# Optimization experiments

Hardware: AMD Instinct MI355X
Metric: run time of the kernel (lower is better)

The kernel has to match this reference:

```python
import jax, jax.numpy as jnp
import numpy as np


def gat(feat_src, feat_dst, src, dst, W, al, ar, b):
    # DGL GATConv in eval mode: shared fc for src/dst, additive attention,
    # leaky_relu(0.2), edge-softmax per destination node, elu activation, bias.
    H, D = al.shape
    nd = feat_dst.shape[0]
    hs = (feat_src @ W).reshape(-1, H, D)  # [Ns,H,D]
    hd = (feat_dst @ W).reshape(-1, H, D)  # [Nd,H,D]
    el = (hs * al).sum(-1)  # [Ns,H]
    er = (hd * ar).sum(-1)  # [Nd,H]
    e = jax.nn.leaky_relu(el[src] + er[dst], 0.2)  # [E,H]
    m = jax.lax.stop_gradient(jax.ops.segment_max(e, dst, num_segments=nd))
    a = jnp.exp(e - m[dst])
    s = jax.ops.segment_sum(a, dst, num_segments=nd)
    den = s[dst]
    alpha = a / jnp.where(den == 0, 1.0, den)  # allow_zero_in_degree
    rst = jax.ops.segment_sum(alpha[:, :, None] * hs[src], dst, num_segments=nd)
    return jax.nn.elu(rst + b.reshape(H, D))  # [Nd,H,D]


def setup_inputs():
    key = jax.random.key(0)
    ks = jax.random.split(key, 40)
    NP, NQ, NK, NA = 50000, 20000, 30000, 5000
    EM, EQ, EK, EA = 1600000, 200000, 200000, 100000
    IN, ATT, HID, H, OUT = 128, 64, 32, 4, 1000
    w = lambda k, sh: jax.random.normal(k, sh, jnp.float32) * 0.05
    ri = lambda k, e, n: jax.random.randint(k, (e,), 0, n, dtype=jnp.int32)
    d = dict(
        hp=jax.random.normal(ks[0], (NP, IN), jnp.float32),
        hq=jax.random.normal(ks[1], (NQ, ATT), jnp.float32),
        hk=jax.random.normal(ks[2], (NK, ATT), jnp.float32),
        ha=jax.random.normal(ks[3], (NA, ATT), jnp.float32),
        meta_src=ri(ks[4], EM, NP), meta_dst=ri(ks[5], EM, NP),
        q_src=ri(ks[6], EQ, NQ), q_dst=ri(ks[7], EQ, NP),
        k_src=ri(ks[8], EK, NK), k_dst=ri(ks[9], EK, NP),
        a_src=ri(ks[10], EA, NA), a_dst=ri(ks[11], EA, NP),
        W0=w(ks[12], (IN, H * HID)), al0=w(ks[13], (H, HID)), ar0=w(ks[14], (H, HID)), b0=jnp.zeros((H * HID,), jnp.float32),
        W1=w(ks[15], (H * HID, H * HID)), al1=w(ks[16], (H, HID)), ar1=w(ks[17], (H, HID)), b1=jnp.zeros((H * HID,), jnp.float32),
        Wq=w(ks[18], (64, H * 128)), alq=w(ks[19], (H, 128)), arq=w(ks[20], (H, 128)), bq=jnp.zeros((H * 128,), jnp.float32),
        Wkw=w(ks[21], (64, H * 128)), alkw=w(ks[22], (H, 128)), arkw=w(ks[23], (H, 128)), bkw=jnp.zeros((H * 128,), jnp.float32),
        Watt=w(ks[24], (64, H * 128)), alatt=w(ks[25], (H, 128)), aratt=w(ks[26], (H, 128)), batt=jnp.zeros((H * 128,), jnp.float32),
        Wpnn_a=w(ks[27], (IN, 64)), Wpn_a=w(ks[28], (ATT, 64)),
        Wpnn=w(ks[29], (H * HID, 64)), Wpn=w(ks[30], (H * 128, 64)),
        Wpred=w(ks[31], (256, OUT)), bpred=jnp.zeros((OUT,), jnp.float32),
    )
    return d


def reference(hp, hq, hk, ha, meta_src, meta_dst, q_src, q_dst, k_src, k_dst, a_src, a_dst, W0, al0, ar0, b0, W1, al1, ar1, b1, Wq, alq, arq, bq, Wkw, alkw, arkw, bkw, Watt, alatt, aratt, batt, Wpnn_a, Wpn_a, Wpnn, Wpn, Wpred, bpred):
    NP = hp.shape[0]
    # two pnn_layers over the single used metapath graph (index 1 is skipped in the original)
    h = gat(hp, hp, meta_src, meta_dst, W0, al0, ar0, b0).reshape(NP, -1)  # [NP,128]
    h = gat(h, h, meta_src, meta_dst, W1, al1, ar1, b1).reshape(NP, -1)    # [NP,128]
    hpd = hp @ Wpnn_a  # proj_pnn_a(hp_cache) -> dst features for bipartite GATs
    oq = gat(hq @ Wpn_a, hpd, q_src, q_dst, Wq, alq, arq, bq).reshape(NP, -1)      # [NP,512]
    ok = gat(hk @ Wpn_a, hpd, k_src, k_dst, Wkw, alkw, arkw, bkw).reshape(NP, -1)  # [NP,512]
    oa = gat(ha @ Wpn_a, hpd, a_src, a_dst, Watt, alatt, aratt, batt).reshape(NP, -1)  # [NP,512]
    hcat = jnp.concatenate([h @ Wpnn, oq @ Wpn, ok @ Wpn, oa @ Wpn], axis=1)  # [NP,256]
    return hcat @ Wpred + bpred
```

## Files before the change

kernel.cpp:

```cpp
#include <hip/hip_runtime.h>
#include <hip/hip_bf16.h>
#include <math.h>
#include <stdint.h>

typedef __attribute__((ext_vector_type(8))) short bh8;
typedef __attribute__((ext_vector_type(4))) float f32x4;

#define AS1(p) ((const __attribute__((address_space(1))) void*)(p))
#define AS3(p) ((__attribute__((address_space(3))) void*)(p))

__device__ inline ushort f2b(float f){
  uint u = __builtin_bit_cast(uint, f);
  u += 0x7fff + ((u >> 16) & 1);
  return (ushort)(u >> 16);
}
__device__ inline float b2f(ushort b){ return __builtin_bit_cast(float, (uint)b << 16); }

__global__ void fill_zero_i32(int* __restrict__ p, int n){
  int i = blockIdx.x*blockDim.x + threadIdx.x;
  if(i < n) p[i] = 0;
}

struct P4 { const int* src; const int* dst; uint* ebuf; int* cnt; int E; int cap; int bbeg; int bend; };

__global__ __launch_bounds__(256) void partition_all_k(P4 g0, P4 g1, P4 g2, P4 g3,
    int* __restrict__ bcur, int range){
  P4 G; int gi;
  int b = blockIdx.x;
  if(b < g0.bend){ G = g0; gi = 0; }
  else if(b < g1.bend){ G = g1; gi = 1; }
  else if(b < g2.bend){ G = g2; gi = 2; }
  else { G = g3; gi = 3; }
  const int lb = b - G.bbeg, nb = G.bend - G.bbeg;
  __shared__ int hist[8], base[8];
  const int tid = threadIdx.x;
  int* bc = bcur + gi*8;
  for(int c0 = lb*256; c0 < G.E; c0 += nb*256){
    int i = c0 + tid;
    int d = 0, s = 0, bk = -1;
    if(i < G.E){ d = G.dst[i]; s = G.src[i]; bk = d / range; }
    if(tid < 8) hist[tid] = 0;
    __syncthreads();
    int rank = 0;
    if(bk >= 0){
      rank = atomicAdd(&hist[bk], 1);
      atomicAdd(&G.cnt[d], 1);
    }
    __syncthreads();
    if(tid < 8) base[tid] = hist[tid] ? atomicAdd(&bc[tid], hist[tid]) : 0;
    __syncthreads();
    if(bk >= 0){
      int pos = base[bk] + rank;
      if(pos < G.cap) G.ebuf[(size_t)bk*G.cap + pos] = ((uint)s << 13) | (uint)(d - bk*range);
    }
    __syncthreads();
  }
}

struct SB4 { const uint* ebuf; int cap; int* cursor; int* colv; int bbeg; int bend; };
__global__ __launch_bounds__(256) void scatter_all_k(SB4 g0, SB4 g1, SB4 g2, SB4 g3,
    const int* __restrict__ bcur, int range){
  SB4 G; int gi;
  int b = blockIdx.x;
  if(b < g0.bend){ G = g0; gi = 0; }
  else if(b < g1.bend){ G = g1; gi = 1; }
  else if(b < g2.bend){ G = g2; gi = 2; }
  else { G = g3; gi = 3; }
  const int local = b - G.bbeg, J = (G.bend - G.bbeg) >> 3;
  const int bk = local & 7, j = local >> 3;
  int nb = bcur[gi*8 + bk]; if(nb > G.cap) nb = G.cap;
  const uint* eb = G.ebuf + (size_t)bk*G.cap;
  int* ub = G.cursor + bk*range;
  int per = (nb + J - 1)/J;
  int beg = j*per, end = beg + per; if(end > nb) end = nb;
  for(int i = beg + threadIdx.x; i < end; i += 256){
    uint e = eb[i];
    int p = atomicAdd(&ub[e & 8191u], 1);
    G.colv[p] = (int)(e >> 13);
  }
}

__global__ __launch_bounds__(1024) void scan4_k(
    const int* c0, const int* c1, const int* c2, const int* c3,
    int* o0, int* o1, int* o2, int* o3,
    int* u0, int* u1, int* u2, int* u3, int n){
  const int* cnt = blockIdx.x==0?c0:(blockIdx.x==1?c1:(blockIdx.x==2?c2:c3));
  int* ofs    = blockIdx.x==0?o0:(blockIdx.x==1?o1:(blockIdx.x==2?o2:o3));
  int* cursor = blockIdx.x==0?u0:(blockIdx.x==1?u1:(blockIdx.x==2?u2:u3));
  __shared__ int wsum[16];
  __shared__ int carry_s;
  int tid = threadIdx.x, wid = tid >> 6, lane = tid & 63;
  if(tid == 0) carry_s = 0;
  __syncthreads();
  for(int base = 0; base < n; base += 4096){
    int i0 = base + tid*4;
    int4 v = make_int4(0,0,0,0);
    if(i0 + 3 < n) v = *(const int4*)(cnt + i0);
    else if(i0 < n){
      v.x = cnt[i0];
      if(i0+1 < n) v.y = cnt[i0+1];
      if(i0+2 < n) v.z = cnt[i0+2];
    }
    int s1 = v.x + v.y, s2 = s1 + v.z, tot = s2 + v.w;
    int x = tot;
    #pragma unroll
    for(int off = 1; off < 64; off <<= 1){
      int t = __shfl_up(x, off);
      if(lane >= off) x += t;
    }
    if(lane == 63) wsum[wid] = x;
    __syncthreads();
    if(tid < 16){
      int y = wsum[tid];
      #pragma unroll
      for(int off = 1; off < 16; off <<= 1){
        int t = __shfl_up(y, off);
        if(tid >= off) y += t;
      }
      wsum[tid] = y;
    }
    __syncthreads();
    int pre = (wid ? wsum[wid-1] : 0) + carry_s + (x - tot);
    if(i0 + 3 < n){
      int4 o = make_int4(pre, pre+v.x, pre+s1, pre+s2);
      *(int4*)(ofs + i0) = o;
      *(int4*)(cursor + i0) = o;
    } else if(i0 < n){
      ofs[i0] = pre; cursor[i0] = pre;
      if(i0+1 < n){ ofs[i0+1] = pre+v.x; cursor[i0+1] = pre+v.x; }
      if(i0+2 < n){ ofs[i0+2] = pre+s1; cursor[i0+2] = pre+s1; }
    }
    __syncthreads();
    if(tid == 0) carry_s += wsum[15];
    __syncthreads();
  }
  if(tid == 0) ofs[n] = carry_s;
}

__global__ void cvt_all_k(const float* i0, const float* i1, const float* i2, const float* i3,
    ushort* o0, ushort* o1, ushort* o2, ushort* o3, int4 cum){
  int i = blockIdx.x*blockDim.x + threadIdx.x;
  const float* in; ushort* out; int base;
  if(i < cum.x){ in=i0; out=o0; base=0; }
  else if(i < cum.y){ in=i1; out=o1; base=cum.x; }
  else if(i < cum.z){ in=i2; out=o2; base=cum.y; }
  else if(i < cum.w){ in=i3; out=o3; base=cum.z; }
  else return;
  int l = i - base;
  float4 v = ((const float4*)in)[l];
  ushort4 o; o.x=f2b(v.x); o.y=f2b(v.y); o.z=f2b(v.z); o.w=f2b(v.w);
  ((ushort4*)out)[l] = o;
}

struct WTD { const float* W; ushort* WT; int K; int N; };
struct WTAll { WTD d[7]; int cum[8]; };
__global__ void wT_all_k(WTAll a){
  int idx = blockIdx.x*blockDim.x + threadIdx.x;
  if(idx >= a.cum[7]) return;
  int j = 0;
  #pragma unroll
  for(int t = 1; t < 7; t++) if(idx >= a.cum[t]) j = t;
  int l = idx - a.cum[j];
  WTD d = a.d[j];
  int n = l / d.K, k = l - n*d.K;
  d.WT[l] = (n < d.N) ? f2b(d.W[(size_t)k*d.N + n]) : (ushort)0;
}

__global__ void wTg3_k(const float* W0, const float* W1, const float* W2, ushort* WT){
  int idx = blockIdx.x*blockDim.x + threadIdx.x;
  if(idx >= 3*32768) return;
  int g = idx >> 15, rem = idx & 32767;
  const float* W = g==0 ? W0 : (g==1 ? W1 : W2);
  int h = rem >> 13, r2 = rem & 8191;
  int n = r2 >> 6, k = r2 & 63;
  WT[idx] = f2b(W[(size_t)k*512 + h*128 + n]);
}

struct FD { const float* W; const float* a; float* out; int K; int D; };
struct FAll { FD d[10]; };
__global__ void fold_all_k(FAll f){
  FD d = f.d[blockIdx.x];
  for(int i = threadIdx.x; i < d.K*4; i += 256){
    int k = i >> 2, h = i & 3;
    const float* wr = d.W + (size_t)k*4*d.D + (size_t)h*d.D;
    const float* ar = d.a + (size_t)h*d.D;
    float s = 0.f;
    for(int dd = 0; dd < d.D; dd++) s += wr[dd]*ar[dd];
    d.out[i] = s;
  }
}

__device__ inline void ld4v(const float* p, float* v){
  float4 t = *(const float4*)p; v[0]=t.x; v[1]=t.y; v[2]=t.z; v[3]=t.w;
}
__device__ inline void ld4v(const ushort* p, float* v){
  ushort4 t = *(const ushort4*)p; v[0]=b2f(t.x); v[1]=b2f(t.y); v[2]=b2f(t.z); v[3]=b2f(t.w);
}

__global__ __launch_bounds__(256) void gemv4v_seg3(const ushort* __restrict__ A,
    const float* __restrict__ W0, const float* __restrict__ W1, const float* __restrict__ W2,
    float* __restrict__ outv, int M, int b1, int b2){
  const int w = (blockIdx.x*blockDim.x + threadIdx.x) >> 6;
  const int lane = threadIdx.x & 63;
  const int r = lane >> 4, q = lane & 15;
  int row = w*4 + r;
  bool valid = row < M;
  int rowc = valid ? row : (M-1);
  const float* Wf = rowc < b1 ? W0 : (rowc < b2 ? W1 : W2);
  float av[4];
  ld4v(A + (size_t)rowc*64 + q*4, av);
  float a[4] = {0.f,0.f,0.f,0.f};
  #pragma unroll
  for(int kk = 0; kk < 4; kk++){
    float4 wv = *(const float4*)(Wf + (q*4+kk)*4);
    a[0] += av[kk]*wv.x; a[1] += av[kk]*wv.y; a[2] += av[kk]*wv.z; a[3] += av[kk]*wv.w;
  }
  #pragma unroll
  for(int off = 1; off < 16; off <<= 1){
    a[0] += __shfl_xor(a[0], off); a[1] += __shfl_xor(a[1], off);
    a[2] += __shfl_xor(a[2], off); a[3] += __shfl_xor(a[3], off);
  }
  if(valid && q == 0){
    float4 o; o.x=a[0]; o.y=a[1]; o.z=a[2]; o.w=a[3];
    *(float4*)(outv + (size_t)row*4) = o;
  }
}

__global__ __launch_bounds__(256) void gemv4v_er3(const ushort* __restrict__ A,
    const float* __restrict__ W0, const float* __restrict__ W1, const float* __restrict__ W2,
    float* __restrict__ o0, float* __restrict__ o1, float* __restrict__ o2, int M){
  const int w = (blockIdx.x*blockDim.x + threadIdx.x) >> 6;
  const int lane = threadIdx.x & 63;
  const int r = lane >> 4, q = lane & 15;
  int row = w*4 + r;
  bool valid = row < M;
  int rowc = valid ? row : (M-1);
  float av[4];
  ld4v(A + (size_t)rowc*64 + q*4, av);
  float a[12];
  #pragma unroll
  for(int t = 0; t < 12; t++) a[t] = 0.f;
  #pragma unroll
  for(int kk = 0; kk < 4; kk++){
    float4 w0 = *(const float4*)(W0 + (q*4+kk)*4);
    float4 w1 = *(const float4*)(W1 + (q*4+kk)*4);
    float4 w2 = *(const float4*)(W2 + (q*4+kk)*4);
    a[0] += av[kk]*w0.x; a[1] += av[kk]*w0.y; a[2] += av[kk]*w0.z; a[3] += av[kk]*w0.w;
    a[4] += av[kk]*w1.x; a[5] += av[kk]*w1.y; a[6] += av[kk]*w1.z; a[7] += av[kk]*w1.w;
    a[8] += av[kk]*w2.x; a[9] += av[kk]*w2.y; a[10]+= av[kk]*w2.z; a[11]+= av[kk]*w2.w;
  }
  #pragma unroll
  for(int off = 1; off < 16; off <<= 1)
    #pragma unroll
    for(int t = 0; t < 12; t++) a[t] += __shfl_xor(a[t], off);
  if(valid && q == 0){
    float4 x; x.x=a[0]; x.y=a[1]; x.z=a[2]; x.w=a[3];
    *(float4*)(o0 + (size_t)row*4) = x;
    float4 y; y.x=a[4]; y.y=a[5]; y.z=a[6]; y.w=a[7];
    *(float4*)(o1 + (size_t)row*4) = y;
    float4 z; z.x=a[8]; z.y=a[9]; z.z=a[10]; z.w=a[11];
    *(float4*)(o2 + (size_t)row*4) = z;
  }
}

template<typename T>
__global__ __launch_bounds__(256) void gemv8v(const T* __restrict__ A,
    const float* __restrict__ Wfa, const float* __restrict__ Wfb,
    float* __restrict__ oa, float* __restrict__ ob, int M, int lda){
  const int w = (blockIdx.x*blockDim.x + threadIdx.x) >> 6;
  const int lane = threadIdx.x & 63;
  const int r = lane >> 5, q = lane & 31;
  int row = w*2 + r;
  bool valid = row < M;
  int rowc = valid ? row : (M-1);
  float av[4];
  ld4v(A + (size_t)rowc*lda + q*4, av);
  float a[4] = {0.f,0.f,0.f,0.f}, b[4] = {0.f,0.f,0.f,0.f};
  #pragma unroll
  for(int kk = 0; kk < 4; kk++){
    float4 wa = *(const float4*)(Wfa + (q*4+kk)*4);
    float4 wb = *(const float4*)(Wfb + (q*4+kk)*4);
    a[0] += av[kk]*wa.x; a[1] += av[kk]*wa.y; a[2] += av[kk]*wa.z; a[3] += av[kk]*wa.w;
    b[0] += av[kk]*wb.x; b[1] += av[kk]*wb.y; b[2] += av[kk]*wb.z; b[3] += av[kk]*wb.w;
  }
  #pragma unroll
  for(int off = 1; off < 32; off <<= 1){
    a[0] += __shfl_xor(a[0], off); a[1] += __shfl_xor(a[1], off);
    a[2] += __shfl_xor(a[2], off); a[3] += __shfl_xor(a[3], off);
    b[0] += __shfl_xor(b[0], off); b[1] += __shfl_xor(b[1], off);
    b[2] += __shfl_xor(b[2], off); b[3] += __shfl_xor(b[3], off);
  }
  if(valid && q == 0){
    float4 o; o.x=a[0]; o.y=a[1]; o.z=a[2]; o.w=a[3];
    *(float4*)(oa + (size_t)row*4) = o;
    float4 p; p.x=b[0]; p.y=b[1]; p.z=b[2]; p.w=b[3];
    *(float4*)(ob + (size_t)row*4) = p;
  }
}

struct GSeg { const ushort* A; const ushort* BT; const float* bias; void* C; int ldc; };

template<int BN, typename OutT, bool BIAS>
__global__ __launch_bounds__(256) void gemm_mfma_b(GSeg s0, GSeg s1, GSeg s2,
    int M, int N, int K, int lda){
  constexpr int BM = 128, BK = 64;
  constexpr int NI = BN/32;
  constexpr int AIT = BM*BK/(256*8);
  constexpr int BIT = BN*BK/(256*8);
  __shared__ ushort lds[BM*BK + BN*BK];
  ushort* ldsA = lds;
  ushort* ldsB = lds + BM*BK;
  GSeg S = blockIdx.z == 0 ? s0 : (blockIdx.z == 1 ? s1 : s2);
  const int tid = threadIdx.x, wid = tid >> 6, lane = tid & 63;
  const int wr = wid >> 1, wc = wid & 1;
  const int rowbase = blockIdx.x*BM;
  const int colbase = blockIdx.y*BN;

  f32x4 acc[4][NI];
  #pragma unroll
  for(int mi = 0; mi < 4; mi++)
    #pragma unroll
    for(int ni = 0; ni < NI; ni++) acc[mi][ni] = (f32x4)0.f;

  for(int k0 = 0; k0 < K; k0 += BK){
    #pragma unroll
    for(int it = 0; it < AIT; it++){
      int idx = it*256 + wid*64 + lane;
      int r = idx >> 3, sl = idx & 7;
      int kb = sl ^ (r & 7);
      int grow = rowbase + r; if(grow >= M) grow = M-1;
      const ushort* src = S.A + (size_t)grow*lda + k0 + kb*8;
      __builtin_amdgcn_global_load_lds(AS1(src), AS3(ldsA + (size_t)(it*256 + wid*64)*8), 16, 0, 0);
    }
    #pragma unroll
    for(int it = 0; it < BIT; it++){
      int idx = it*256 + wid*64 + lane;
      int r = idx >> 3, sl = idx & 7;
      int kb = sl ^ (r & 7);
      const ushort* src = S.BT + (size_t)(colbase + r)*K + k0 + kb*8;
      __builtin_amdgcn_global_load_lds(AS1(src), AS3(ldsB + (size_t)(it*256 + wid*64)*8), 16, 0, 0);
    }
    __syncthreads();
    #pragma unroll
    for(int kk = 0; kk < 2; kk++){
      bh8 af[4], bf[NI];
      #pragma unroll
      for(int mi = 0; mi < 4; mi++){
        int arow = wr*64 + mi*16 + (lane & 15);
        int kb = kk*4 + (lane >> 4);
        af[mi] = *(const bh8*)(ldsA + arow*BK + ((kb ^ (arow & 7)) << 3));
      }
      #pragma unroll
      for(int ni = 0; ni < NI; ni++){
        int brow = wc*(BN/2) + ni*16 + (lane & 15);
        int kb = kk*4 + (lane >> 4);
        bf[ni] = *(const bh8*)(ldsB + brow*BK + ((kb ^ (brow & 7)) << 3));
      }
      #pragma unroll
      for(int mi = 0; mi < 4; mi++)
        #pragma unroll
        for(int ni = 0; ni < NI; ni++)
          acc[mi][ni] = __builtin_amdgcn_mfma_f32_16x16x32_bf16(af[mi], bf[ni], acc[mi][ni], 0, 0, 0);
    }
    __syncthreads();
  }
  OutT* C = (OutT*)S.C;
  #pragma unroll
  for(int mi = 0; mi < 4; mi++){
    #pragma unroll
    for(int ni = 0; ni < NI; ni++){
      int col = colbase + wc*(BN/2) + ni*16 + (lane & 15);
      if(col >= N) continue;
      float bv = BIAS ? S.bias[col] : 0.f;
      #pragma unroll
      for(int j = 0; j < 4; j++){
        int row = rowbase + wr*64 + mi*16 + (lane >> 4)*4 + j;
        if(row >= M) continue;
        float v = acc[mi][ni][j] + bv;
        if constexpr (sizeof(OutT) == 4) C[(size_t)row*S.ldc + col] = v;
        else                             C[(size_t)row*S.ldc + col] = (OutT)f2b(v);
      }
    }
  }
}

__global__ __launch_bounds__(256) void bip_tail_k(
    const ushort* __restrict__ agg,
    const ushort* __restrict__ WTg3,
    const ushort* __restrict__ WpnT,
    const float* bias0, const float* bias1, const float* bias2,
    ushort* __restrict__ hcat,
    int M){
  __shared__ ushort ldsA[128*64];
  __shared__ ushort ldsB[128*64];
  __shared__ ushort ldsP[128*128];
  __shared__ ushort ldsW[64*128];
  const int seg = blockIdx.z;
  const ushort* A  = agg + (size_t)seg*M*256;
  const ushort* Wg = WTg3 + (size_t)seg*32768;
  const float* bias = seg==0 ? bias0 : (seg==1 ? bias1 : bias2);
  ushort* outp = hcat + 64 + seg*64;
  const int tid = threadIdx.x, lane = tid & 63, wid = tid >> 6;
  const int wr = wid >> 1, wc = wid & 1;
  const int rowbase = blockIdx.x*128;

  f32x4 acc_out[4][2];
  #pragma unroll
  for(int mi = 0; mi < 4; mi++){ acc_out[mi][0] = (f32x4)0.f; acc_out[mi][1] = (f32x4)0.f; }

  for(int hh = 0; hh < 4; hh++){
    #pragma unroll
    for(int it = 0; it < 4; it++){
      int idx = it*256 + tid;
      int r = idx >> 3, sl = idx & 7;
      int kb = sl ^ (r & 7);
      int grow = rowbase + r; if(grow >= M) grow = M-1;
      __builtin_amdgcn_global_load_lds(AS1(A + (size_t)grow*256 + hh*64 + kb*8),
                                       AS3(ldsA + (size_t)idx*8), 16, 0, 0);
    }
    #pragma unroll
    for(int it = 0; it < 4; it++){
      int idx = it*256 + tid;
      int r = idx >> 3, sl = idx & 7;
      int kb = sl ^ (r & 7);
      __builtin_amdgcn_global_load_lds(AS1(Wg + hh*8192 + r*64 + kb*8),
                                       AS3(ldsB + (size_t)idx*8), 16, 0, 0);
    }
    #pragma unroll
    for(int it = 0; it < 4; it++){
      int idx = it*256 + tid;
      int r = idx >> 4, sl = idx & 15;
      int kb = sl ^ (r & 7);
      __builtin_amdgcn_global_load_lds(AS1(WpnT + (size_t)r*512 + hh*128 + kb*8),
                                       AS3(ldsW + (size_t)idx*8), 16, 0, 0);
    }
    __syncthreads();
    f32x4 accp[4][4];
    #pragma unroll
    for(int mi = 0; mi < 4; mi++)
      #pragma unroll
      for(int ni = 0; ni < 4; ni++) accp[mi][ni] = (f32x4)0.f;
    #pragma unroll
    for(int kk = 0; kk < 2; kk++){
      bh8 af[4], bf[4];
      int kb = kk*4 + (lane >> 4);
      #pragma unroll
      for(int mi = 0; mi < 4; mi++){
        int arow = wr*64 + mi*16 + (lane & 15);
        af[mi] = *(const bh8*)(ldsA + arow*64 + ((kb ^ (arow & 7)) << 3));
      }
      #pragma unroll
      for(int ni = 0; ni < 4; ni++){
        int brow = wc*64 + ni*16 + (lane & 15);
        bf[ni] = *(const bh8*)(ldsB + brow*64 + ((kb ^ (brow & 7)) << 3));
      }
      #pragma unroll
      for(int mi = 0; mi < 4; mi++)
        #pragma unroll
        for(int ni = 0; ni < 4; ni++)
          accp[mi][ni] = __builtin_amdgcn_mfma_f32_16x16x32_bf16(af[mi], bf[ni], accp[mi][ni], 0, 0, 0);
    }
    #pragma unroll
    for(int mi = 0; mi < 4; mi++)
      #pragma unroll
      for(int ni = 0; ni < 4; ni++){
        int col = wc*64 + ni*16 + (lane & 15);
        float bv = bias[hh*128 + col];
        int rbase = wr*64 + mi*16 + (lane >> 4)*4;
        #pragma unroll
        for(int j = 0; j < 4; j++){
          float v = accp[mi][ni][j] + bv;
          v = v > 0.f ? v : (__expf(v) - 1.f);
          int row = rbase + j;
          ldsP[row*128 + ((((col >> 3) ^ (row & 7))) << 3) + (col & 7)] = f2b(v);
        }
      }
    __syncthreads();
    #pragma unroll
    for(int kk = 0; kk < 4; kk++){
      bh8 af[4], bf[2];
      int kb = kk*4 + (lane >> 4);
      #pragma unroll
      for(int mi = 0; mi < 4; mi++){
        int arow = wr*64 + mi*16 + (lane & 15);
        af[mi] = *(const bh8*)(ldsP + arow*128 + ((kb ^ (arow & 7)) << 3));
      }
      #pragma unroll
      for(int ni = 0; ni < 2; ni++){
        int brow = wc*32 + ni*16 + (lane & 15);
        bf[ni] = *(const bh8*)(ldsW + brow*128 + ((kb ^ (brow & 7)) << 3));
      }
      #pragma unroll
      for(int mi = 0; mi < 4; mi++)
        #pragma unroll
        for(int ni = 0; ni < 2; ni++)
          acc_out[mi][ni] = __builtin_amdgcn_mfma_f32_16x16x32_bf16(af[mi], bf[ni], acc_out[mi][ni], 0, 0, 0);
    }
    __syncthreads();
  }
  #pragma unroll
  for(int mi = 0; mi < 4; mi++)
    #pragma unroll
    for(int ni = 0; ni < 2; ni++){
      int col = wc*32 + ni*16 + (lane & 15);
      #pragma unroll
      for(int j = 0; j < 4; j++){
        int row = rowbase + wr*64 + mi*16 + (lane >> 4)*4 + j;
        if(row >= M) continue;
        outp[(size_t)row*256 + col] = f2b(acc_out[mi][ni][j]);
      }
    }
}

__global__ __launch_bounds__(256) void gat_agg_meta(
    const ushort* __restrict__ hs, const float* __restrict__ el,
    const float* __restrict__ er, const int* __restrict__ ofs,
    const int* __restrict__ colv, const float* __restrict__ bias,
    ushort* __restrict__ outv, int Nd){
  const int wslot = threadIdx.x >> 6;
  const int node = blockIdx.x*4 + wslot;
  const int lane = threadIdx.x & 63;
  __shared__ int   lds_s[4][64];
  __shared__ float lds_w[4][256];
  if(node >= Nd) return;
  const int e0 = ofs[node], e1 = ofs[node+1];
  const int g = lane >> 4, q = lane & 15;
  const int hh = q >> 2;
  const float4 erv = *(const float4*)(er + (size_t)node*4);
  float m0=-INFINITY, m1=-INFINITY, m2=-INFINITY, m3=-INFINITY;
  float sw0=0.f, sw1=0.f, sw2=0.f, sw3=0.f;
  float acc[8];
  #pragma unroll
  for(int r = 0; r < 8; r++) acc[r] = 0.f;

  for(int base = e0; base < e1; base += 64){
    int nch = e1 - base; if(nch > 64) nch = 64;
    int s_l = colv[base + (lane < nch ? lane : nch-1)];
    float4 ev = *(const float4*)(el + (size_t)s_l*4);
    float x0 = ev.x + erv.x; x0 = x0 > 0.f ? x0 : 0.2f*x0;
    float x1 = ev.y + erv.y; x1 = x1 > 0.f ? x1 : 0.2f*x1;
    float x2 = ev.z + erv.z; x2 = x2 > 0.f ? x2 : 0.2f*x2;
    float x3 = ev.w + erv.w; x3 = x3 > 0.f ? x3 : 0.2f*x3;
    if(lane >= nch){ x0 = x1 = x2 = x3 = -INFINITY; }
    float c0=x0, c1=x1, c2=x2, c3=x3;
    #pragma unroll
    for(int off = 32; off; off >>= 1){
      c0 = fmaxf(c0, __shfl_xor(c0, off));
      c1 = fmaxf(c1, __shfl_xor(c1, off));
      c2 = fmaxf(c2, __shfl_xor(c2, off));
      c3 = fmaxf(c3, __shfl_xor(c3, off));
    }
    float n0 = fmaxf(m0,c0), n1 = fmaxf(m1,c1), n2 = fmaxf(m2,c2), n3 = fmaxf(m3,c3);
    float r0 = __expf(m0-n0), r1 = __expf(m1-n1), r2 = __expf(m2-n2), r3 = __expf(m3-n3);
    float w0 = __expf(x0-n0), w1 = __expf(x1-n1), w2 = __expf(x2-n2), w3 = __expf(x3-n3);
    sw0 = sw0*r0 + w0; sw1 = sw1*r1 + w1; sw2 = sw2*r2 + w2; sw3 = sw3*r3 + w3;
    float rh = hh==0 ? r0 : (hh==1 ? r1 : (hh==2 ? r2 : r3));
    #pragma unroll
    for(int r = 0; r < 8; r++) acc[r] *= rh;
    m0=n0; m1=n1; m2=n2; m3=n3;
    lds_s[wslot][lane] = s_l;
    lds_w[wslot][lane*4+0] = w0; lds_w[wslot][lane*4+1] = w1;
    lds_w[wslot][lane*4+2] = w2; lds_w[wslot][lane*4+3] = w3;
    int npad = (nch + 15) & ~15;
    for(int j = 0; j < npad; j += 16){
      int sv[4]; float wv[4];
      #pragma unroll
      for(int u = 0; u < 4; u++){
        sv[u] = lds_s[wslot][j + u*4 + g];
        wv[u] = lds_w[wslot][(j + u*4 + g)*4 + hh];
      }
      bh8 vv[4];
      #pragma unroll
      for(int u = 0; u < 4; u++)
        vv[u] = *(const bh8*)(hs + (size_t)sv[u]*128 + q*8);
      #pragma unroll
      for(int u = 0; u < 4; u++)
        #pragma unroll
        for(int r = 0; r < 8; r++) acc[r] += wv[u] * b2f((ushort)vv[u][r]);
    }
  }
  #pragma unroll
  for(int off = 32; off; off >>= 1){
    sw0 += __shfl_xor(sw0, off); sw1 += __shfl_xor(sw1, off);
    sw2 += __shfl_xor(sw2, off); sw3 += __shfl_xor(sw3, off);
  }
  #pragma unroll
  for(int r = 0; r < 8; r++){
    acc[r] += __shfl_xor(acc[r], 16);
    acc[r] += __shfl_xor(acc[r], 32);
  }
  float swh = hh==0 ? sw0 : (hh==1 ? sw1 : (hh==2 ? sw2 : sw3));
  float den = (swh == 0.f) ? 1.f : swh;
  if(g == 0){
    bh8 ov;
    #pragma unroll
    for(int r = 0; r < 8; r++){
      float v = acc[r]/den + bias[q*8 + r];
      v = v > 0.f ? v : (__expf(v) - 1.f);
      ov[r] = (short)f2b(v);
    }
    *(bh8*)(outv + (size_t)node*128 + q*8) = ov;
  }
}

struct ASeg { const int* ofs; const int* colv; const float* el; const float* er; ushort* agg; };
__global__ __launch_bounds__(256) void gat_agg_proj3(ASeg s0, ASeg s1, ASeg s2,
    const ushort* __restrict__ proj, int2 pbase, int Nd, int nb){
  const int seg = blockIdx.x / nb;
  const ASeg S = seg == 0 ? s0 : (seg == 1 ? s1 : s2);
  const ushort* pj = proj + (size_t)(seg == 0 ? 0 : (seg == 1 ? pbase.x : pbase.y))*64;
  const int node = (blockIdx.x - seg*nb)*16 + (threadIdx.x >> 4);
  const int q = threadIdx.x & 15;
  if(node >= Nd) return;
  const int e0 = S.ofs[node], e1 = S.ofs[node+1];
  const int deg = e1 - e0;
  const float4 erv = *(const float4*)(S.er + (size_t)node*4);
  float sw0=0.f, sw1=0.f, sw2=0.f, sw3=0.f;
  float acc[4][4];
  #pragma unroll
  for(int d = 0; d < 4; d++)
    #pragma unroll
    for(int h = 0; h < 4; h++) acc[d][h] = 0.f;

  if(deg <= 8){
    const int ebase = (deg > 0) ? e0 : 0;
    int sv[8];
    #pragma unroll
    for(int u = 0; u < 8; u++) sv[u] = S.colv[ebase + (u < deg ? u : 0)];
    float xa[8], xb[8], xc[8], xd[8];
    #pragma unroll
    for(int u = 0; u < 8; u++){
      float4 ev = *(const float4*)(S.el + (size_t)sv[u]*4);
      float t0 = ev.x + erv.x; xa[u] = t0 > 0.f ? t0 : 0.2f*t0;
      float t1 = ev.y + erv.y; xb[u] = t1 > 0.f ? t1 : 0.2f*t1;
      float t2 = ev.z + erv.z; xc[u] = t2 > 0.f ? t2 : 0.2f*t2;
      float t3 = ev.w + erv.w; xd[u] = t3 > 0.f ? t3 : 0.2f*t3;
    }
    float m0=-INFINITY, m1=-INFINITY, m2=-INFINITY, m3=-INFINITY;
    #pragma unroll
    for(int u = 0; u < 8; u++) if(u < deg){
      m0 = fmaxf(m0, xa[u]); m1 = fmaxf(m1, xb[u]);
      m2 = fmaxf(m2, xc[u]); m3 = fmaxf(m3, xd[u]);
    }
    ushort4 pv[8];
    #pragma unroll
    for(int u = 0; u < 8; u++) pv[u] = *(const ushort4*)(pj + (size_t)sv[u]*64 + q*4);
    #pragma unroll
    for(int u = 0; u < 8; u++) if(u < deg){
      float w0 = __expf(xa[u]-m0), w1 = __expf(xb[u]-m1);
      float w2 = __expf(xc[u]-m2), w3 = __expf(xd[u]-m3);
      sw0 += w0; sw1 += w1; sw2 += w2; sw3 += w3;
      float f0 = b2f(pv[u].x), f1 = b2f(pv[u].y), f2 = b2f(pv[u].z), f3 = b2f(pv[u].w);
      acc[0][0] += w0*f0; acc[0][1] += w1*f0; acc[0][2] += w2*f0; acc[0][3] += w3*f0;
      acc[1][0] += w0*f1; acc[1][1] += w1*f1; acc[1][2] += w2*f1; acc[1][3] += w3*f1;
      acc[2][0] += w0*f2; acc[2][1] += w1*f2; acc[2][2] += w2*f2; acc[2][3] += w3*f2;
      acc[3][0] += w0*f3; acc[3][1] += w1*f3; acc[3][2] += w2*f3; acc[3][3] += w3*f3;
    }
  } else {
    float m0=-INFINITY, m1=-INFINITY, m2=-INFINITY, m3=-INFINITY;
    for(int e = e0; e < e1; e++){
      int s = S.colv[e];
      float4 ev = *(const float4*)(S.el + (size_t)s*4);
      float x0 = ev.x + erv.x; x0 = x0 > 0.f ? x0 : 0.2f*x0;
      float x1 = ev.y + erv.y; x1 = x1 > 0.f ? x1 : 0.2f*x1;
      float x2 = ev.z + erv.z; x2 = x2 > 0.f ? x2 : 0.2f*x2;
      float x3 = ev.w + erv.w; x3 = x3 > 0.f ? x3 : 0.2f*x3;
      m0 = fmaxf(m0,x0); m1 = fmaxf(m1,x1); m2 = fmaxf(m2,x2); m3 = fmaxf(m3,x3);
    }
    for(int e = e0; e < e1; e++){
      int s = S.colv[e];
      float4 ev = *(const float4*)(S.el + (size_t)s*4);
      float x0 = ev.x + erv.x; x0 = x0 > 0.f ? x0 : 0.2f*x0;
      float x1 = ev.y + erv.y; x1 = x1 > 0.f ? x1 : 0.2f*x1;
      float x2 = ev.z + erv.z; x2 = x2 > 0.f ? x2 : 0.2f*x2;
      float x3 = ev.w + erv.w; x3 = x3 > 0.f ? x3 : 0.2f*x3;
      float w0 = __expf(x0-m0), w1 = __expf(x1-m1);
      float w2 = __expf(x2-m2), w3 = __expf(x3-m3);
      sw0 += w0; sw1 += w1; sw2 += w2; sw3 += w3;
      ushort4 p = *(const ushort4*)(pj + (size_t)s*64 + q*4);
      float f0 = b2f(p.x), f1 = b2f(p.y), f2 = b2f(p.z), f3 = b2f(p.w);
      acc[0][0] += w0*f0; acc[0][1] += w1*f0; acc[0][2] += w2*f0; acc[0][3] += w3*f0;
      acc[1][0] += w0*f1; acc[1][1] += w1*f1; acc[1][2] += w2*f1; acc[1][3] += w3*f1;
      acc[2][0] += w0*f2; acc[2][1] += w1*f2; acc[2][2] += w2*f2; acc[2][3] += w3*f2;
      acc[3][0] += w0*f3; acc[3][1] += w1*f3; acc[3][2] += w2*f3; acc[3][3] += w3*f3;
    }
  }
  float dn[4];
  dn[0] = (sw0 == 0.f) ? 1.f : sw0;
  dn[1] = (sw1 == 0.f) ? 1.f : sw1;
  dn[2] = (sw2 == 0.f) ? 1.f : sw2;
  dn[3] = (sw3 == 0.f) ? 1.f : sw3;
  ushort* orow = S.agg + (size_t)node*256;
  #pragma unroll
  for(int h = 0; h < 4; h++){
    ushort4 o;
    o.x = f2b(acc[0][h]/dn[h]); o.y = f2b(acc[1][h]/dn[h]);
    o.z = f2b(acc[2][h]/dn[h]); o.w = f2b(acc[3][h]/dn[h]);
    *(ushort4*)(orow + h*64 + q*4) = o;
  }
}

extern "C" void kernel_launch(void* const* d_in, const int* in_sizes, int n_in,
                              void* d_out, int out_size, void* d_ws, size_t ws_size,
                              hipStream_t stream){
  const float* hp   = (const float*)d_in[0];
  const float* hq   = (const float*)d_in[1];
  const float* hk   = (const float*)d_in[2];
  const float* ha   = (const float*)d_in[3];
  const int* meta_src = (const int*)d_in[4];
  const int* meta_dst = (const int*)d_in[5];
  const int* q_src = (const int*)d_in[6];
  const int* q_dst = (const int*)d_in[7];
  const int* k_src = (const int*)d_in[8];
  const int* k_dst = (const int*)d_in[9];
  const int* a_src = (const int*)d_in[10];
  const int* a_dst = (const int*)d_in[11];
  const float* W0  = (const float*)d_in[12]; const float* al0 = (const float*)d_in[13];
  const float* ar0 = (const float*)d_in[14]; const float* b0  = (const float*)d_in[15];
  const float* W1  = (const float*)d_in[16]; const float* al1 = (const float*)d_in[17];
  const float* ar1 = (const float*)d_in[18]; const float* b1  = (const float*)d_in[19];
  const float* Wq  = (const float*)d_in[20]; const float* alq = (const float*)d_in[21];
  const float* arq = (const float*)d_in[22]; const float* bq  = (const float*)d_in[23];
  const float* Wkw = (const float*)d_in[24]; const float* alkw= (const float*)d_in[25];
  const float* arkw= (const float*)d_in[26]; const float* bkw = (const float*)d_in[27];
  const float* Watt= (const float*)d_in[28]; const float* alatt=(const float*)d_in[29];
  const float* aratt=(const float*)d_in[30]; const float* batt= (const float*)d_in[31];
  const float* Wpnn_a = (const float*)d_in[32];
  const float* Wpn_a  = (const float*)d_in[33];
  const float* Wpnn   = (const float*)d_in[34];
  const float* Wpn    = (const float*)d_in[35];
  const float* Wpred  = (const float*)d_in[36];
  const float* bpred  = (const float*)d_in[37];
  (void)n_in; (void)out_size; (void)ws_size;

  const int IN = 128, ATT = 64;
  const int NP = in_sizes[0]/IN, NQ = in_sizes[1]/ATT, NK = in_sizes[2]/ATT, NA = in_sizes[3]/ATT;
  const int EM = in_sizes[4], EQ = in_sizes[6], EK = in_sizes[8], EA = in_sizes[10];
  const int range = (NP + 7)/8;
  const int NS = NQ + NK + NA;

  uint8_t* wp = (uint8_t*)d_ws;
  auto alloc = [&](size_t bytes)->uint8_t*{
    uint8_t* p = wp; wp += (bytes + 255) & ~(size_t)255; return p;
  };
  ushort* hcat_b = (ushort*)alloc((size_t)NP*256*2);
  ushort* hbuf_b = (ushort*)alloc((size_t)NP*128*2);
  ushort* hp_b   = (ushort*)alloc((size_t)NP*128*2);
  ushort* hpd_b  = (ushort*)alloc((size_t)NP*64*2);
  ushort* hs_b   = (ushort*)alloc((size_t)NP*128*2);
  ushort* feat_all = (ushort*)alloc((size_t)NS*64*2);
  ushort* proj_all = (ushort*)alloc((size_t)NS*64*2);
  ushort* agg_all  = (ushort*)alloc((size_t)3*NP*256*2);
  float* el    = (float*)alloc((size_t)NP*4*4);
  float* er    = (float*)alloc((size_t)NP*4*4);
  float* el_all= (float*)alloc((size_t)NS*4*4);
  float* er_all= (float*)alloc((size_t)3*NP*4*4);
  float* wf    = (float*)alloc((size_t)10*512*4);
  int* cnt4    = (int*)alloc((size_t)(4*NP+32)*4);
  int* bcur    = cnt4 + 4*NP;
  int* cur4    = (int*)alloc((size_t)4*NP*4);
  int* ofsm    = (int*)alloc((size_t)(NP+4)*4);
  int* ofsq    = (int*)alloc((size_t)(NP+4)*4);
  int* ofsk    = (int*)alloc((size_t)(NP+4)*4);
  int* ofsa    = (int*)alloc((size_t)(NP+4)*4);
  int* colm    = (int*)alloc((size_t)EM*4);
  int* colq    = (int*)alloc((size_t)EQ*4);
  int* colk    = (int*)alloc((size_t)EK*4);
  int* cola    = (int*)alloc((size_t)EA*4);
  const int capM = EM/4+1024, capQ = EQ/4+1024, capK = EK/4+1024, capA = EA/4+1024;
  uint* ebm = (uint*)alloc((size_t)8*capM*4);
  uint* ebq = (uint*)alloc((size_t)8*capQ*4);
  uint* ebk = (uint*)alloc((size_t)8*capK*4);
  uint* eba = (uint*)alloc((size_t)8*capA*4);
  ushort* W0T    = (ushort*)alloc(128*128*2);
  ushort* W1T    = (ushort*)alloc(128*128*2);
  ushort* WTg3   = (ushort*)alloc((size_t)3*4*128*64*2);
  ushort* WpnT   = (ushort*)alloc((size_t)64*512*2);
  ushort* WpnnT  = (ushort*)alloc(64*128*2);
  ushort* Wpnn_aT= (ushort*)alloc(64*128*2);
  ushort* Wpn_aT = (ushort*)alloc(64*64*2);
  ushort* WpredT = (ushort*)alloc((size_t)1024*256*2);

  fill_zero_i32<<<(4*NP+32+255)/256, 256, 0, stream>>>(cnt4, 4*NP+32);
  {
    int bm = EM/1024 + 1, bq2 = EQ/1024 + 1, bk2 = EK/1024 + 1, ba2 = EA/1024 + 1;
    P4 g0{meta_src, meta_dst, ebm, cnt4 + 0*NP, EM, capM, 0, bm};
    P4 g1{q_src, q_dst, ebq, cnt4 + 1*NP, EQ, capQ, bm, bm+bq2};
    P4 g2{k_src, k_dst, ebk, cnt4 + 2*NP, EK, capK, bm+bq2, bm+bq2+bk2};
    P4 g3{a_src, a_dst, eba, cnt4 + 3*NP, EA, capA, bm+bq2+bk2, bm+bq2+bk2+ba2};
    partition_all_k<<<g3.bend, 256, 0, stream>>>(g0, g1, g2, g3, bcur, range);
  }
  auto Jof = [&](int E){ int J = E/65536 + 8; if(J > 48) J = 48; return J; };
  {
    scan4_k<<<4, 1024, 0, stream>>>(cnt4, cnt4+NP, cnt4+2*NP, cnt4+3*NP,
                                    ofsm, ofsq, ofsk, ofsa,
                                    cur4, cur4+NP, cur4+2*NP, cur4+3*NP, NP);
    int jm = 8*Jof(EM), jq = 8*Jof(EQ), jk = 8*Jof(EK), ja = 8*Jof(EA);
    SB4 s0{ebm, capM, cur4 + 0*NP, colm, 0, jm};
    SB4 s1{ebq, capQ, cur4 + 1*NP, colq, jm, jm+jq};
    SB4 s2{ebk, capK, cur4 + 2*NP, colk, jm+jq, jm+jq+jk};
    SB4 s3{eba, capA, cur4 + 3*NP, cola, jm+jq+jk, jm+jq+jk+ja};
    scatter_all_k<<<s3.bend, 256, 0, stream>>>(s0, s1, s2, s3, bcur, range);
  }

  {
    int c0 = NP*128/4, c1 = c0 + NQ*64/4, c2 = c1 + NK*64/4, c3 = c2 + NA*64/4;
    cvt_all_k<<<(c3+255)/256, 256, 0, stream>>>(hp, hq, hk, ha,
        hp_b, feat_all, feat_all + (size_t)NQ*64, feat_all + (size_t)(NQ+NK)*64,
        make_int4(c0, c1, c2, c3));
  }
  {
    WTAll a;
    a.d[0] = {W0, W0T, 128, 128};      a.d[1] = {W1, W1T, 128, 128};
    a.d[2] = {Wpn, WpnT, 512, 64};     a.d[3] = {Wpnn, WpnnT, 128, 64};
    a.d[4] = {Wpnn_a, Wpnn_aT, 128, 64}; a.d[5] = {Wpn_a, Wpn_aT, 64, 64};
    a.d[6] = {Wpred, WpredT, 256, 1000};
    int items[7] = {128*128, 128*128, 64*512, 64*128, 64*128, 64*64, 1024*256};
    a.cum[0] = 0;
    for(int t = 0; t < 7; t++) a.cum[t+1] = a.cum[t] + items[t];
    wT_all_k<<<(a.cum[7]+255)/256, 256, 0, stream>>>(a);
  }
  wTg3_k<<<(3*32768+255)/256, 256, 0, stream>>>(Wq, Wkw, Watt, WTg3);
  {
    FAll f;
    f.d[0] = {W0, al0, wf+0*512, 128, 32};  f.d[1] = {W0, ar0, wf+1*512, 128, 32};
    f.d[2] = {W1, al1, wf+2*512, 128, 32};  f.d[3] = {W1, ar1, wf+3*512, 128, 32};
    f.d[4] = {Wq, alq, wf+4*512, 64, 128};  f.d[5] = {Wq, arq, wf+5*512, 64, 128};
    f.d[6] = {Wkw, alkw, wf+6*512, 64, 128};f.d[7] = {Wkw, arkw, wf+7*512, 64, 128};
    f.d[8] = {Watt, alatt, wf+8*512, 64, 128};f.d[9] = {Watt, aratt, wf+9*512, 64, 128};
    fold_all_k<<<10, 256, 0, stream>>>(f);
  }

  auto launch_gemm = [&]<int BN, typename OutT, bool BIAS>(
      GSeg a, GSeg b, GSeg c, int nseg, int M, int N, int K, int lda){
    int Npad = (N + BN - 1)/BN*BN;
    dim3 g((M + 127)/128, Npad/BN, nseg);
    gemm_mfma_b<BN, OutT, BIAS><<<g, 256, 0, stream>>>(a, b, c, M, N, K, lda);
  };
  GSeg z{};

  launch_gemm.template operator()<128, ushort, false>(
      GSeg{hp_b, W0T, nullptr, hs_b, 128}, z, z, 1, NP, 128, 128, 128);
  gemv8v<ushort><<<(NP/2+3)/4, 256, 0, stream>>>(hp_b, wf+0*512, wf+1*512, el, er, NP, 128);
  gat_agg_meta<<<(NP+3)/4, 256, 0, stream>>>(hs_b, el, er, ofsm, colm, b0, hbuf_b, NP);

  launch_gemm.template operator()<128, ushort, false>(
      GSeg{hbuf_b, W1T, nullptr, hs_b, 128}, z, z, 1, NP, 128, 128, 128);
  gemv8v<ushort><<<(NP/2+3)/4, 256, 0, stream>>>(hbuf_b, wf+2*512, wf+3*512, el, er, NP, 128);
  gat_agg_meta<<<(NP+3)/4, 256, 0, stream>>>(hs_b, el, er, ofsm, colm, b1, hbuf_b, NP);

  launch_gemm.template operator()<64, ushort, false>(
      GSeg{hbuf_b, WpnnT, nullptr, hcat_b, 256},
      GSeg{hp_b, Wpnn_aT, nullptr, hpd_b, 64}, z, 2, NP, 64, 128, 128);

  launch_gemm.template operator()<64, ushort, false>(
      GSeg{feat_all, Wpn_aT, nullptr, proj_all, 64}, z, z, 1, NS, 64, 64, 64);
  gemv4v_seg3<<<(NS/4+3)/4, 256, 0, stream>>>(proj_all, wf+4*512, wf+6*512, wf+8*512,
      el_all, NS, NQ, NQ+NK);
  gemv4v_er3<<<(NP/4+3)/4, 256, 0, stream>>>(hpd_b, wf+5*512, wf+7*512, wf+9*512,
      er_all, er_all + (size_t)NP*4, er_all + (size_t)2*NP*4, NP);
  {
    int nb = (NP+15)/16;
    ASeg a0{ofsq, colq, el_all,                    er_all,                    agg_all};
    ASeg a1{ofsk, colk, el_all + (size_t)NQ*4,     er_all + (size_t)NP*4,     agg_all + (size_t)NP*256};
    ASeg a2{ofsa, cola, el_all + (size_t)(NQ+NK)*4,er_all + (size_t)2*NP*4,   agg_all + (size_t)2*NP*256};
    gat_agg_proj3<<<3*nb, 256, 0, stream>>>(a0, a1, a2, proj_all, make_int2(NQ, NQ+NK), NP, nb);
  }
  {
    dim3 g((NP+127)/128, 1, 3);
    bip_tail_k<<<g, 256, 0, stream>>>(agg_all, WTg3, WpnT, bq, bkw, batt, hcat_b, NP);
  }

  launch_gemm.template operator()<128, float, true>(
      GSeg{hcat_b, WpredT, bpred, d_out, 1000}, z, z, 1, NP, 1000, 256, 256);
}
```

Before: 758.2 us.

## Move per-node degree counting from global atomics to LDS histograms over buckets

The partition kernel no longer does a global atomicAdd per edge on the destination count array. It now handles 2048 edges per block with vectorised int4 loads and per-wave LDS bucket histograms, and the bucket cursors are padded to separate cache lines. A new kernel builds per-bucket node histograms in shared memory from the partitioned edge buffer and writes them as J partial rows. The scan kernel sums those partials before its prefix scan. This removes contended global atomics and the large zero-fill, at the cost of an extra kernel launch and extra partial-count traffic.

Result: faster. 715.5 us (-5.6%).

```diff
diff --git a/kernel.cpp b/kernel.cpp
--- a/kernel.cpp
+++ b/kernel.cpp
@@ -8,6 +8,7 @@
 
 #define AS1(p) ((const __attribute__((address_space(1))) void*)(p))
 #define AS3(p) ((__attribute__((address_space(3))) void*)(p))
+#define PSL 2048
 
 __device__ inline ushort f2b(float f){
   uint u = __builtin_bit_cast(uint, f);
@@ -21,7 +22,7 @@
   if(i < n) p[i] = 0;
 }
 
-struct P4 { const int* src; const int* dst; uint* ebuf; int* cnt; int E; int cap; int bbeg; int bend; };
+struct P4 { const int* src; const int* dst; uint* ebuf; int E; int cap; int bbeg; int bend; };
 
 __global__ __launch_bounds__(256) void partition_all_k(P4 g0, P4 g1, P4 g2, P4 g3,
     int* __restrict__ bcur, int range){
@@ -31,30 +32,77 @@
   else if(b < g1.bend){ G = g1; gi = 1; }
   else if(b < g2.bend){ G = g2; gi = 2; }
   else { G = g3; gi = 3; }
-  const int lb = b - G.bbeg, nb = G.bend - G.bbeg;
-  __shared__ int hist[8], base[8];
-  const int tid = threadIdx.x;
-  int* bc = bcur + gi*8;
-  for(int c0 = lb*256; c0 < G.E; c0 += nb*256){
-    int i = c0 + tid;
-    int d = 0, s = 0, bk = -1;
-    if(i < G.E){ d = G.dst[i]; s = G.src[i]; bk = d / range; }
-    if(tid < 8) hist[tid] = 0;
-    __syncthreads();
-    int rank = 0;
-    if(bk >= 0){
-      rank = atomicAdd(&hist[bk], 1);
-      atomicAdd(&G.cnt[d], 1);
-    }
-    __syncthreads();
-    if(tid < 8) base[tid] = hist[tid] ? atomicAdd(&bc[tid], hist[tid]) : 0;
-    __syncthreads();
-    if(bk >= 0){
-      int pos = base[bk] + rank;
-      if(pos < G.cap) G.ebuf[(size_t)bk*G.cap + pos] = ((uint)s << 13) | (uint)(d - bk*range);
-    }
-    __syncthreads();
-  }
+  const int beg = (b - G.bbeg)*PSL;
+  const int tid = threadIdx.x, w = tid >> 6;
+  __shared__ int hist4[4][8];
+  __shared__ int cur4[4][8];
+  if(tid < 32) (&hist4[0][0])[tid] = 0;
+  __syncthreads();
+  int dv[8], sv[8], bv[8];
+  const int bi = beg + tid*8;
+  if(beg + PSL <= G.E){
+    int4 d0 = *(const int4*)(G.dst + bi);
+    int4 d1 = *(const int4*)(G.dst + bi + 4);
+    int4 s0 = *(const int4*)(G.src + bi);
+    int4 s1 = *(const int4*)(G.src + bi + 4);
+    dv[0]=d0.x; dv[1]=d0.y; dv[2]=d0.z; dv[3]=d0.w;
+    dv[4]=d1.x; dv[5]=d1.y; dv[6]=d1.z; dv[7]=d1.w;
+    sv[0]=s0.x; sv[1]=s0.y; sv[2]=s0.z; sv[3]=s0.w;
+    sv[4]=s1.x; sv[5]=s1.y; sv[6]=s1.z; sv[7]=s1.w;
+    #pragma unroll
+    for(int u = 0; u < 8; u++) bv[u] = dv[u]/range;
+  } else {
+    #pragma unroll
+    for(int u = 0; u < 8; u++){
+      int i = bi + u;
+      bool ok = i < G.E;
+      dv[u] = ok ? G.dst[i] : 0;
+      sv[u] = ok ? G.src[i] : 0;
+      bv[u] = ok ? dv[u]/range : -1;
+    }
+  }
+  #pragma unroll
+  for(int u = 0; u < 8; u++) if(bv[u] >= 0) atomicAdd(&hist4[w][bv[u]], 1);
+  __syncthreads();
+  if(tid < 8){
+    int h0 = hist4[0][tid], h1 = hist4[1][tid], h2 = hist4[2][tid], h3 = hist4[3][tid];
+    int tot = h0 + h1 + h2 + h3;
+    int bs = tot ? atomicAdd(&bcur[(gi*8 + tid)*16], tot) : 0;
+    cur4[0][tid] = bs;
+    cur4[1][tid] = bs + h0;
+    cur4[2][tid] = bs + h0 + h1;
+    cur4[3][tid] = bs + h0 + h1 + h2;
+  }
+  __syncthreads();
+  #pragma unroll
+  for(int u = 0; u < 8; u++) if(bv[u] >= 0){
+    int pos = atomicAdd(&cur4[w][bv[u]], 1);
+    if(pos < G.cap) G.ebuf[(size_t)bv[u]*G.cap + pos] = ((uint)sv[u] << 13) | (uint)(dv[u] - bv[u]*range);
+  }
+}
+
+struct H4 { const uint* ebuf; int cap; };
+__global__ __launch_bounds__(256) void hist_all_k(H4 h0, H4 h1, H4 h2, H4 h3,
+    const int* __restrict__ bcur, int* __restrict__ part,
+    int range, int NPL, int J, int NP){
+  __shared__ int h[8192];
+  const int x = blockIdx.x;
+  const int g = x/(8*J);
+  const int rem = x - g*8*J;
+  const int bk = rem/J, j = rem - bk*J;
+  H4 H = g==0 ? h0 : (g==1 ? h1 : (g==2 ? h2 : h3));
+  for(int i = threadIdx.x; i < range; i += 256) h[i] = 0;
+  __syncthreads();
+  int nb = bcur[(g*8 + bk)*16]; if(nb > H.cap) nb = H.cap;
+  const uint* eb = H.ebuf + (size_t)bk*H.cap;
+  int per = (nb + J - 1)/J;
+  int lo = j*per, hi = lo + per; if(hi > nb) hi = nb;
+  for(int i = lo + threadIdx.x; i < hi; i += 256)
+    atomicAdd(&h[eb[i] & 8191u], 1);
+  __syncthreads();
+  int lim = NP - bk*range; if(lim > range) lim = range;
+  int* dst = part + ((size_t)g*J + j)*NPL + bk*range;
+  for(int i = threadIdx.x; i < lim; i += 256) dst[i] = h[i];
 }
 
 struct SB4 { const uint* ebuf; int cap; int* cursor; int* colv; int bbeg; int bend; };
@@ -68,7 +116,7 @@
   else { G = g3; gi = 3; }
   const int local = b - G.bbeg, J = (G.bend - G.bbeg) >> 3;
   const int bk = local & 7, j = local >> 3;
-  int nb = bcur[gi*8 + bk]; if(nb > G.cap) nb = G.cap;
+  int nb = bcur[(gi*8 + bk)*16]; if(nb > G.cap) nb = G.cap;
   const uint* eb = G.ebuf + (size_t)bk*G.cap;
   int* ub = G.cursor + bk*range;
   int per = (nb + J - 1)/J;
@@ -81,10 +129,10 @@
 }
 
 __global__ __launch_bounds__(1024) void scan4_k(
-    const int* c0, const int* c1, const int* c2, const int* c3,
+    const int* __restrict__ part, int J, int NPL,
     int* o0, int* o1, int* o2, int* o3,
     int* u0, int* u1, int* u2, int* u3, int n){
-  const int* cnt = blockIdx.x==0?c0:(blockIdx.x==1?c1:(blockIdx.x==2?c2:c3));
+  const int* pg = part + (size_t)blockIdx.x*J*NPL;
   int* ofs    = blockIdx.x==0?o0:(blockIdx.x==1?o1:(blockIdx.x==2?o2:o3));
   int* cursor = blockIdx.x==0?u0:(blockIdx.x==1?u1:(blockIdx.x==2?u2:u3));
   __shared__ int wsum[16];
@@ -95,11 +143,17 @@
   for(int base = 0; base < n; base += 4096){
     int i0 = base + tid*4;
     int4 v = make_int4(0,0,0,0);
-    if(i0 + 3 < n) v = *(const int4*)(cnt + i0);
-    else if(i0 < n){
-      v.x = cnt[i0];
-      if(i0+1 < n) v.y = cnt[i0+1];
-      if(i0+2 < n) v.z = cnt[i0+2];
+    if(i0 + 3 < n){
+      for(int j = 0; j < J; j++){
+        int4 t = *(const int4*)(pg + (size_t)j*NPL + i0);
+        v.x += t.x; v.y += t.y; v.z += t.z; v.w += t.w;
+      }
+    } else if(i0 < n){
+      for(int j = 0; j < J; j++){
+        v.x += pg[(size_t)j*NPL + i0];
+        if(i0+1 < n) v.y += pg[(size_t)j*NPL + i0+1];
+        if(i0+2 < n) v.z += pg[(size_t)j*NPL + i0+2];
+      }
     }
     int s1 = v.x + v.y, s2 = s1 + v.z, tot = s2 + v.w;
     int x = tot;
@@ -385,12 +439,10 @@
 }
 
 __global__ __launch_bounds__(256) void bip_tail_k(
-    const ushort* __restrict__ agg,
-    const ushort* __restrict__ WTg3,
+    const ushort* __restrict__ agg, const ushort* __restrict__ WTg3,
     const ushort* __restrict__ WpnT,
     const float* bias0, const float* bias1, const float* bias2,
-    ushort* __restrict__ hcat,
-    int M){
+    ushort* __restrict__ hcat, int M){
   __shared__ ushort ldsA[128*64];
   __shared__ ushort ldsB[128*64];
   __shared__ ushort ldsP[128*128];
@@ -738,6 +790,8 @@
   const int EM = in_sizes[4], EQ = in_sizes[6], EK = in_sizes[8], EA = in_sizes[10];
   const int range = (NP + 7)/8;
   const int NS = NQ + NK + NA;
+  const int JH = 8;
+  const int NPL = (NP + 3) & ~3;
 
   uint8_t* wp = (uint8_t*)d_ws;
   auto alloc = [&](size_t bytes)->uint8_t*{
@@ -756,8 +810,8 @@
   float* el_all= (float*)alloc((size_t)NS*4*4);
   float* er_all= (float*)alloc((size_t)3*NP*4*4);
   float* wf    = (float*)alloc((size_t)10*512*4);
-  int* cnt4    = (int*)alloc((size_t)(4*NP+32)*4);
-  int* bcur    = cnt4 + 4*NP;
+  int* bcur    = (int*)alloc((size_t)512*4);
+  int* part    = (int*)alloc((size_t)4*JH*NPL*4);
   int* cur4    = (int*)alloc((size_t)4*NP*4);
   int* ofsm    = (int*)alloc((size_t)(NP+4)*4);
   int* ofsq    = (int*)alloc((size_t)(NP+4)*4);
@@ -781,20 +835,22 @@
   ushort* Wpn_aT = (ushort*)alloc(64*64*2);
   ushort* WpredT = (ushort*)alloc((size_t)1024*256*2);
 
-  fill_zero_i32<<<(4*NP+32+255)/256, 256, 0, stream>>>(cnt4, 4*NP+32);
+  fill_zero_i32<<<2, 256, 0, stream>>>(bcur, 512);
   {
-    int bm = EM/1024 + 1, bq2 = EQ/1024 + 1, bk2 = EK/1024 + 1, ba2 = EA/1024 + 1;
-    P4 g0{meta_src, meta_dst, ebm, cnt4 + 0*NP, EM, capM, 0, bm};
-    P4 g1{q_src, q_dst, ebq, cnt4 + 1*NP, EQ, capQ, bm, bm+bq2};
-    P4 g2{k_src, k_dst, ebk, cnt4 + 2*NP, EK, capK, bm+bq2, bm+bq2+bk2};
-    P4 g3{a_src, a_dst, eba, cnt4 + 3*NP, EA, capA, bm+bq2+bk2, bm+bq2+bk2+ba2};
+    int bm = (EM+PSL-1)/PSL, bq2 = (EQ+PSL-1)/PSL, bk2 = (EK+PSL-1)/PSL, ba2 = (EA+PSL-1)/PSL;
+    P4 g0{meta_src, meta_dst, ebm, EM, capM, 0, bm};
+    P4 g1{q_src, q_dst, ebq, EQ, capQ, bm, bm+bq2};
+    P4 g2{k_src, k_dst, ebk, EK, capK, bm+bq2, bm+bq2+bk2};
+    P4 g3{a_src, a_dst, eba, EA, capA, bm+bq2+bk2, bm+bq2+bk2+ba2};
     partition_all_k<<<g3.bend, 256, 0, stream>>>(g0, g1, g2, g3, bcur, range);
   }
-  auto Jof = [&](int E){ int J = E/65536 + 8; if(J > 48) J = 48; return J; };
   {
-    scan4_k<<<4, 1024, 0, stream>>>(cnt4, cnt4+NP, cnt4+2*NP, cnt4+3*NP,
+    H4 h0{ebm, capM}, h1{ebq, capQ}, h2{ebk, capK}, h3{eba, capA};
+    hist_all_k<<<4*8*JH, 256, 0, stream>>>(h0, h1, h2, h3, bcur, part, range, NPL, JH, NP);
+    scan4_k<<<4, 1024, 0, stream>>>(part, JH, NPL,
                                     ofsm, ofsq, ofsk, ofsa,
                                     cur4, cur4+NP, cur4+2*NP, cur4+3*NP, NP);
+    auto Jof = [&](int E){ int J = E/65536 + 8; if(J > 48) J = 48; return J; };
     int jm = 8*Jof(EM), jq = 8*Jof(EQ), jk = 8*Jof(EK), ja = 8*Jof(EA);
     SB4 s0{ebm, capM, cur4 + 0*NP, colm, 0, jm};
     SB4 s1{ebq, capQ, cur4 + 1*NP, colq, jm, jm+jq};
```
